# Performance work log

Measured on AMD Instinct MI355X. Metric: run time of the kernel, lower is better.

The kernel has to match this reference:

```python
import jax, jax.numpy as jnp
import numpy as np

B, K_IN, K_STATE, K_OUT = 16384, 256, 1024, 256
MEANDT = 1.0


def setup_inputs() -> dict:
    key = jax.random.key(0)
    ks = jax.random.split(key, 12)
    stdv = 1.0 / np.sqrt(K_STATE)
    u = lambda k, shape: jax.random.uniform(k, shape, jnp.float32, -stdv, stdv)
    # Lh_gate bias: second half (r-gate) initialized to -1 per init_params
    b_hg = jnp.concatenate([u(ks[6], (K_STATE,)), -jnp.ones((K_STATE,), jnp.float32)])
    return {
        "x": jax.random.normal(ks[0], (B, K_IN), jnp.float32),
        "state": jax.random.normal(ks[1], (B, K_STATE), jnp.float32),
        "dt": jnp.full((1,), 0.1, jnp.float32),
        "W_in": u(ks[2], (K_STATE, K_IN)),   # expand_input Linear weight
        "b_in": u(ks[3], (K_STATE,)),
        "W_lx": u(ks[4], (3 * K_STATE, K_STATE)),  # Lx, no bias
        "W_hg": u(ks[5], (2 * K_STATE, K_STATE)),  # Lh_gate
        "b_hg": b_hg,
        "W_hl": u(ks[7], (K_STATE, K_STATE)),      # Lh_lin
        "b_hl": u(ks[8], (K_STATE,)),
        "W_y1": u(ks[9], (K_STATE, K_STATE)),      # Ly first Linear, no bias
        "W_y2": u(ks[10], (K_OUT, K_STATE)),       # Ly second Linear, no bias
    }


def reference(x, state, dt, W_in, b_in, W_lx, W_hg, b_hg, W_hl, b_hl, W_y1, W_y2):
    dt = dt[0]

    def f(x0, h):
        # GRU-like derivative: z * (tanh(Lx_lin + Lh_lin(r*h)) - h) / meandt
        lx = x0 @ W_lx.T                       # [B, 3K]
        lh_gate = h @ W_hg.T + b_hg            # [B, 2K]
        gates = jax.nn.sigmoid(lx[:, : 2 * K_STATE] + lh_gate)
        z = gates[:, :K_STATE]
        r = gates[:, K_STATE:]
        lin = lx[:, 2 * K_STATE:] + (r * h) @ W_hl.T + b_hl
        return z * (jnp.tanh(lin) - h) / MEANDT

    # expand_input: Linear + Tanh. x_half/x_full are None -> all stages use x0.
    x0 = jnp.tanh(x @ W_in.T + b_in)           # [B, K]

    # RK4 integration
    k1 = f(x0, state)
    k2 = f(x0, state + dt * (0.5 * k1))
    k3 = f(x0, state + dt * (0.5 * k2))
    k4 = f(x0, state + dt * k3)
    state_new = state + dt * (k1 + 2 * k2 + 2 * k3 + k4) / 6  # dropout p=0 -> identity

    # Ly: Linear -> Tanh -> Linear (no biases)
    y_new = jnp.tanh(state_new @ W_y1.T) @ W_y2.T              # [B, K_OUT]
    return y_new, state_new
```

## Files before the change

### kernel.cpp

```cpp
#include <hip/hip_runtime.h>
#include <cstdint>
#include <cstddef>

#define DEVI __device__ __forceinline__

namespace {

constexpr int Bsz  = 16384;
constexpr int KIN  = 256;
constexpr int KST  = 1024;
constexpr int KOUT = 256;

typedef __bf16 bf16x8 __attribute__((ext_vector_type(8)));
typedef float  f32x4  __attribute__((ext_vector_type(4)));

DEVI float sigmoidf_(float x) { return 1.0f / (1.0f + expf(-x)); }

DEVI void gload16(const void* gsrc, void* ldst) {
    __builtin_amdgcn_global_load_lds((__attribute__((address_space(1))) void*)gsrc,
                                     (__attribute__((address_space(3))) void*)ldst,
                                     16, 0, 0);
}

DEVI void ld8f(const float* p, float* v) {
    const float4 a = *(const float4*)p;
    const float4 b = *(const float4*)(p + 4);
    v[0]=a.x; v[1]=a.y; v[2]=a.z; v[3]=a.w;
    v[4]=b.x; v[5]=b.y; v[6]=b.z; v[7]=b.w;
}
DEVI void st8f(float* p, const float* v) {
    *(float4*)p       = (float4){v[0],v[1],v[2],v[3]};
    *(float4*)(p + 4) = (float4){v[4],v[5],v[6],v[7]};
}
DEVI void ld8bf(const __bf16* p, float* v) {
    const bf16x8 o = *(const bf16x8*)p;
#pragma unroll
    for (int i = 0; i < 8; ++i) v[i] = (float)o[i];
}
DEVI void st8bf(__bf16* p, const float* v) {
    bf16x8 o;
#pragma unroll
    for (int i = 0; i < 8; ++i) o[i] = (__bf16)v[i];
    *(bf16x8*)p = o;
}
DEVI void ld8h(const float* p, float* v)  { ld8f(p, v); }
DEVI void ld8h(const __bf16* p, float* v) { ld8bf(p, v); }

struct EpX0 {
    __bf16* out; const float* bias;
    DEVI void begin() {}
    DEVI void store16(const float* v, int r, int c) {
#pragma unroll
        for (int q = 0; q < 2; ++q) {
            float b[8], o[8];
            ld8f(bias + c + q * 8, b);
#pragma unroll
            for (int e = 0; e < 8; ++e) o[e] = tanhf(v[q*8+e] + b[e]);
            st8bf(out + (size_t)r * KST + c + q * 8, o);
        }
    }
};
struct EpLx {
    __bf16* out;
    DEVI void begin() {}
    DEVI void store16(const float* v, int r, int c) {
#pragma unroll
        for (int q = 0; q < 2; ++q)
            st8bf(out + (size_t)r * (3 * KST) + c + q * 8, v + q * 8);
    }
};
template <class HT>
struct EpGates {
    __bf16* Z; __bf16* RH; const __bf16* lx; const float* bhg; const HT* h;
    DEVI void begin() {}
    DEVI void store16(const float* v, int r, int c) {
#pragma unroll
        for (int q = 0; q < 2; ++q) {
            float l[8], b[8], g[8];
            ld8bf(lx + (size_t)r * (3 * KST) + c + q * 8, l);
            ld8f(bhg + c + q * 8, b);
#pragma unroll
            for (int e = 0; e < 8; ++e) g[e] = sigmoidf_(l[e] + v[q*8+e] + b[e]);
            if (c < KST) {
                st8bf(Z + (size_t)r * KST + c + q * 8, g);
            } else {
                const size_t i = (size_t)r * KST + (c - KST) + q * 8;
                float hh[8];
                ld8h(h + i, hh);
#pragma unroll
                for (int e = 0; e < 8; ++e) g[e] *= hh[e];
                st8bf(RH + i, g);
            }
        }
    }
};
template <int STAGE, class HT>
struct EpLin {
    const __bf16* Z; const __bf16* lx; const float* bhl; const HT* h;
    const float* state; float* acc; __bf16* hn; const float* dtp;
    float dtv;
    DEVI void begin() { dtv = *dtp; }
    DEVI void store16(const float* v, int r, int c) {
#pragma unroll
        for (int q = 0; q < 2; ++q) {
            const size_t i = (size_t)r * KST + c + q * 8;
            float l[8], z[8], hh[8], st[8], b[8], kk[8], ov[8], hv[8];
            ld8bf(lx + (size_t)r * (3 * KST) + 2 * KST + c + q * 8, l);
            ld8bf(Z + i, z);
            ld8h(h + i, hh);
            ld8f(state + i, st);
            ld8f(bhl + c + q * 8, b);
#pragma unroll
            for (int e = 0; e < 8; ++e)
                kk[e] = z[e] * (tanhf(l[e] + v[q*8+e] + b[e]) - hh[e]);
            if constexpr (STAGE == 0) {
#pragma unroll
                for (int e = 0; e < 8; ++e) { ov[e] = kk[e]; hv[e] = st[e] + 0.5f * dtv * kk[e]; }
            } else if constexpr (STAGE == 1 || STAGE == 2) {
                float a[8]; ld8f(acc + i, a);
                const float hc = (STAGE == 1) ? 0.5f : 1.0f;
#pragma unroll
                for (int e = 0; e < 8; ++e) { ov[e] = a[e] + 2.f * kk[e]; hv[e] = st[e] + hc * dtv * kk[e]; }
            } else {
                float a[8]; ld8f(acc + i, a);
#pragma unroll
                for (int e = 0; e < 8; ++e) { ov[e] = st[e] + dtv * (a[e] + kk[e]) * (1.f / 6.f); hv[e] = ov[e]; }
            }
            st8f(acc + i, ov);
            st8bf(hn + i, hv);
        }
    }
};
struct EpT {
    __bf16* out;
    DEVI void begin() {}
    DEVI void store16(const float* v, int r, int c) {
#pragma unroll
        for (int q = 0; q < 2; ++q) {
            float o[8];
#pragma unroll
            for (int e = 0; e < 8; ++e) o[e] = tanhf(v[q*8+e]);
            st8bf(out + (size_t)r * KST + c + q * 8, o);
        }
    }
};
struct EpY {
    float* out;
    DEVI void begin() {}
    DEVI void store16(const float* v, int r, int c) {
        st8f(out + (size_t)r * KOUT + c, v);
        st8f(out + (size_t)r * KOUT + c + 8, v + 8);
    }
};

template <class Ep>
__global__ __launch_bounds__(256)
void gemm_bt(const __bf16* __restrict__ A, const __bf16* __restrict__ W,
             const int K, Ep ep)
{
    __shared__ __bf16 As[128 * 32];
    __shared__ __bf16 Bs[128 * 32];
    __shared__ float  bounce[32 * 132];
    const int m0 = blockIdx.x * 128;
    const int n0 = blockIdx.y * 128;
    const int t  = threadIdx.x;
    const int l  = t & 63;
    const int w  = t >> 6;
    const int wr = w >> 1;
    const int wc = w & 1;
    const int fr = l & 15;
    const int fq = l >> 4;
    const int srow = t >> 2;
    const int sk   = (t & 3) << 3;

    const __bf16* Ap0 = A + (size_t)(m0 + srow) * K + sk;
    const __bf16* Ap1 = Ap0 + (size_t)64 * K;
    const __bf16* Bp0 = W + (size_t)(n0 + srow) * K + sk;
    const __bf16* Bp1 = Bp0 + (size_t)64 * K;
    __bf16* la0 = &As[t * 8];
    __bf16* la1 = &As[2048 + t * 8];
    __bf16* lb0 = &Bs[t * 8];
    __bf16* lb1 = &Bs[2048 + t * 8];

    f32x4 acc[4][4];
#pragma unroll
    for (int i = 0; i < 4; ++i)
#pragma unroll
        for (int j = 0; j < 4; ++j) acc[i][j] = (f32x4){0.f, 0.f, 0.f, 0.f};

    for (int k0 = 0; k0 < K; k0 += 32) {
        gload16(Ap0 + k0, la0);
        gload16(Ap1 + k0, la1);
        gload16(Bp0 + k0, lb0);
        gload16(Bp1 + k0, lb1);
        __syncthreads();
        bf16x8 av[4], bv[4];
#pragma unroll
        for (int mi = 0; mi < 4; ++mi)
            av[mi] = *(const bf16x8*)&As[(wr * 64 + mi * 16 + fr) * 32 + fq * 8];
#pragma unroll
        for (int ni = 0; ni < 4; ++ni)
            bv[ni] = *(const bf16x8*)&Bs[(wc * 64 + ni * 16 + fr) * 32 + fq * 8];
#pragma unroll
        for (int mi = 0; mi < 4; ++mi)
#pragma unroll
            for (int ni = 0; ni < 4; ++ni)
                acc[mi][ni] = __builtin_amdgcn_mfma_f32_16x16x32_bf16(av[mi], bv[ni], acc[mi][ni], 0, 0, 0);
        __syncthreads();
    }

    ep.begin();
#pragma unroll
    for (int band = 0; band < 4; ++band) {
        if (wr == (band >> 1)) {
            const int mi0 = 2 * (band & 1);
#pragma unroll
            for (int mm = 0; mm < 2; ++mm)
#pragma unroll
                for (int ni = 0; ni < 4; ++ni)
#pragma unroll
                    for (int j = 0; j < 4; ++j)
                        bounce[(mm * 16 + fq * 4 + j) * 132 + wc * 64 + ni * 16 + fr]
                            = acc[mi0 + mm][ni][j];
        }
        __syncthreads();
        {
            const int r  = t >> 3;
            const int c0 = (t & 7) * 16;
            float v[16];
#pragma unroll
            for (int kk = 0; kk < 16; ++kk) v[kk] = bounce[r * 132 + c0 + kk];
            ep.store16(v, m0 + band * 32 + r, n0 + c0);
        }
        __syncthreads();
    }
}

__global__ __launch_bounds__(256)
void cvt_bf16(const float* __restrict__ s, __bf16* __restrict__ d, int n8)
{
    for (int i = blockIdx.x * blockDim.x + threadIdx.x; i < n8; i += gridDim.x * blockDim.x) {
        const float4 a = ((const float4*)s)[2 * i];
        const float4 b = ((const float4*)s)[2 * i + 1];
        bf16x8 v;
        v[0] = (__bf16)a.x; v[1] = (__bf16)a.y; v[2] = (__bf16)a.z; v[3] = (__bf16)a.w;
        v[4] = (__bf16)b.x; v[5] = (__bf16)b.y; v[6] = (__bf16)b.z; v[7] = (__bf16)b.w;
        ((bf16x8*)d)[i] = v;
    }
}

}

extern "C" void kernel_launch(void* const* d_in, const int* in_sizes, int n_in,
                              void* d_out, int out_size, void* d_ws, size_t ws_size,
                              hipStream_t stream)
{
    (void)in_sizes; (void)n_in; (void)out_size;

    const float* x     = (const float*)d_in[0];
    const float* state = (const float*)d_in[1];
    const float* dtp   = (const float*)d_in[2];
    const float* W_in  = (const float*)d_in[3];
    const float* b_in  = (const float*)d_in[4];
    const float* W_lx  = (const float*)d_in[5];
    const float* W_hg  = (const float*)d_in[6];
    const float* b_hg  = (const float*)d_in[7];
    const float* W_hl  = (const float*)d_in[8];
    const float* b_hl  = (const float*)d_in[9];
    const float* W_y1  = (const float*)d_in[10];
    const float* W_y2  = (const float*)d_in[11];

    float* y_out  = (float*)d_out;
    float* st_new = y_out + (size_t)Bsz * KOUT;

    const size_t nWin = (size_t)KST * KIN, nWlx = (size_t)3 * KST * KST,
                 nWhg = (size_t)2 * KST * KST, nWhl = (size_t)KST * KST,
                 nWy1 = (size_t)KST * KST, nWy2 = (size_t)KOUT * KST;
    const size_t fixedB = ((size_t)Bsz * KIN + 2 * (size_t)Bsz * KST
                           + nWin + nWlx + nWhg + nWhl + nWy1 + nWy2) * 2;

    int CB = 1024;
    while (CB < 8192 && fixedB + (size_t)(2 * CB) * KST * 12 <= ws_size) CB <<= 1;
    if (fixedB + (size_t)CB * KST * 12 > ws_size) return;

    uint8_t* p = (uint8_t*)d_ws;
    __bf16* x_bf  = (__bf16*)p; p += (size_t)Bsz * KIN * 2;
    __bf16* st_bf = (__bf16*)p; p += (size_t)Bsz * KST * 2;
    __bf16* snb   = (__bf16*)p; p += (size_t)Bsz * KST * 2;
    __bf16* Wb_in = (__bf16*)p; p += nWin * 2;
    __bf16* Wb_lx = (__bf16*)p; p += nWlx * 2;
    __bf16* Wb_hg = (__bf16*)p; p += nWhg * 2;
    __bf16* Wb_hl = (__bf16*)p; p += nWhl * 2;
    __bf16* Wb_y1 = (__bf16*)p; p += nWy1 * 2;
    __bf16* Wb_y2 = (__bf16*)p; p += nWy2 * 2;
    __bf16* lx    = (__bf16*)p; p += (size_t)CB * 3 * KST * 2;
    __bf16* Zb    = (__bf16*)p; p += (size_t)CB * KST * 2;
    __bf16* h_bf  = (__bf16*)p; p += (size_t)CB * KST * 2;
    __bf16* RH    = (__bf16*)p;
    __bf16* t_bf  = lx;

    const dim3 blk(256);
    auto cg = [](size_t n) { return dim3((unsigned)((n / 8 + 255) / 256 > 2048 ? 2048 : (n / 8 + 255) / 256)); };
    auto g  = [](int M, int N) { return dim3((unsigned)(M / 128), (unsigned)(N / 128)); };

    cvt_bf16<<<cg((size_t)Bsz * KIN), blk, 0, stream>>>(x, x_bf, (int)((size_t)Bsz * KIN / 8));
    cvt_bf16<<<cg((size_t)Bsz * KST), blk, 0, stream>>>(state, st_bf, (int)((size_t)Bsz * KST / 8));
    cvt_bf16<<<cg(nWin), blk, 0, stream>>>(W_in, Wb_in, (int)(nWin / 8));
    cvt_bf16<<<cg(nWlx), blk, 0, stream>>>(W_lx, Wb_lx, (int)(nWlx / 8));
    cvt_bf16<<<cg(nWhg), blk, 0, stream>>>(W_hg, Wb_hg, (int)(nWhg / 8));
    cvt_bf16<<<cg(nWhl), blk, 0, stream>>>(W_hl, Wb_hl, (int)(nWhl / 8));
    cvt_bf16<<<cg(nWy1), blk, 0, stream>>>(W_y1, Wb_y1, (int)(nWy1 / 8));
    cvt_bf16<<<cg(nWy2), blk, 0, stream>>>(W_y2, Wb_y2, (int)(nWy2 / 8));

    for (int c0 = 0; c0 < Bsz; c0 += CB) {
        const __bf16* xs  = x_bf + (size_t)c0 * KIN;
        const __bf16* ssb = st_bf + (size_t)c0 * KST;
        const float*  ss  = state + (size_t)c0 * KST;
        float*  sn   = st_new + (size_t)c0 * KST;
        __bf16* snbs = snb + (size_t)c0 * KST;

        gemm_bt<<<g(CB, KST), blk, 0, stream>>>(xs, Wb_in, KIN, EpX0{h_bf, b_in});
        gemm_bt<<<g(CB, 3 * KST), blk, 0, stream>>>(h_bf, Wb_lx, KST, EpLx{lx});

        gemm_bt<<<g(CB, 2 * KST), blk, 0, stream>>>(ssb, Wb_hg, KST, EpGates<float>{Zb, RH, lx, b_hg, ss});
        gemm_bt<<<g(CB, KST), blk, 0, stream>>>(RH, Wb_hl, KST, EpLin<0, float>{Zb, lx, b_hl, ss, ss, sn, h_bf, dtp});
        gemm_bt<<<g(CB, 2 * KST), blk, 0, stream>>>(h_bf, Wb_hg, KST, EpGates<__bf16>{Zb, RH, lx, b_hg, h_bf});
        gemm_bt<<<g(CB, KST), blk, 0, stream>>>(RH, Wb_hl, KST, EpLin<1, __bf16>{Zb, lx, b_hl, h_bf, ss, sn, h_bf, dtp});
        gemm_bt<<<g(CB, 2 * KST), blk, 0, stream>>>(h_bf, Wb_hg, KST, EpGates<__bf16>{Zb, RH, lx, b_hg, h_bf});
        gemm_bt<<<g(CB, KST), blk, 0, stream>>>(RH, Wb_hl, KST, EpLin<2, __bf16>{Zb, lx, b_hl, h_bf, ss, sn, h_bf, dtp});
        gemm_bt<<<g(CB, 2 * KST), blk, 0, stream>>>(h_bf, Wb_hg, KST, EpGates<__bf16>{Zb, RH, lx, b_hg, h_bf});
        gemm_bt<<<g(CB, KST), blk, 0, stream>>>(RH, Wb_hl, KST, EpLin<3, __bf16>{Zb, lx, b_hl, h_bf, ss, sn, snbs, dtp});
    }

    const int CBY = (4 * CB < Bsz) ? 4 * CB : Bsz;
    for (int c0 = 0; c0 < Bsz; c0 += CBY) {
        gemm_bt<<<g(CBY, KST), blk, 0, stream>>>(snb + (size_t)c0 * KST, Wb_y1, KST, EpT{t_bf});
        gemm_bt<<<g(CBY, KOUT), blk, 0, stream>>>(t_bf, Wb_y2, KST, EpY{y_out + (size_t)c0 * KOUT});
    }
}
```

Measured before the change: 1.539 ms.

## Add 256x256-tile double-buffered GEMM kernel and enlarge batch chunk size

```diff
diff --git a/kernel.cpp b/kernel.cpp
--- a/kernel.cpp
+++ b/kernel.cpp
@@ -152,6 +152,108 @@
         st8f(out + (size_t)r * KOUT + c + 8, v + 8);
     }
 };
+
+DEVI void compute_tile64(const __bf16* a, const __bf16* b,
+                         f32x4 (&acc)[8][4], int wr, int wc, int fr, int fq)
+{
+#pragma unroll
+    for (int kk = 0; kk < 2; ++kk) {
+        bf16x8 av[8], bv[4];
+#pragma unroll
+        for (int mi = 0; mi < 8; ++mi)
+            av[mi] = *(const bf16x8*)&a[(wr * 128 + mi * 16 + fr) * 64 + kk * 32 + fq * 8];
+#pragma unroll
+        for (int ni = 0; ni < 4; ++ni)
+            bv[ni] = *(const bf16x8*)&b[(wc * 64 + ni * 16 + fr) * 64 + kk * 32 + fq * 8];
+#pragma unroll
+        for (int mi = 0; mi < 8; ++mi)
+#pragma unroll
+            for (int ni = 0; ni < 4; ++ni)
+                acc[mi][ni] = __builtin_amdgcn_mfma_f32_16x16x32_bf16(av[mi], bv[ni], acc[mi][ni], 0, 0, 0);
+    }
+}
+
+template <class Ep>
+__global__ __launch_bounds__(512, 2)
+void gemm_bt2(const __bf16* __restrict__ A, const __bf16* __restrict__ W,
+              const int K, Ep ep)
+{
+    __shared__ __bf16 sm[4][256 * 64];
+    const int m0 = blockIdx.x * 256;
+    const int n0 = blockIdx.y * 256;
+    const int t  = threadIdx.x;
+    const int l  = t & 63;
+    const int w  = t >> 6;
+    const int wr = w >> 2;
+    const int wc = w & 3;
+    const int fr = l & 15;
+    const int fq = l >> 4;
+    const int srow = t >> 3;
+    const int scol = (t & 7) << 3;
+
+    const __bf16* Ap = A + (size_t)(m0 + srow) * K + scol;
+    const __bf16* Bp = W + (size_t)(n0 + srow) * K + scol;
+
+    f32x4 acc[8][4];
+#pragma unroll
+    for (int i = 0; i < 8; ++i)
+#pragma unroll
+        for (int j = 0; j < 4; ++j) acc[i][j] = (f32x4){0.f, 0.f, 0.f, 0.f};
+
+    const int NT = K >> 6;
+
+#define STAGE_KT(buf, kt)                                                     \
+    {                                                                         \
+        const int k0_ = (kt) << 6;                                            \
+        __bf16* da_ = &sm[(buf) * 2 + 0][t * 8];                              \
+        __bf16* db_ = &sm[(buf) * 2 + 1][t * 8];                              \
+        _Pragma("unroll")                                                     \
+        for (int q = 0; q < 4; ++q) {                                         \
+            gload16(Ap + (size_t)(q * 64) * K + k0_, da_ + q * 4096);         \
+            gload16(Bp + (size_t)(q * 64) * K + k0_, db_ + q * 4096);         \
+        }                                                                     \
+    }
+
+    STAGE_KT(0, 0);
+    __syncthreads();
+    int cur = 0;
+    for (int kt = 0; kt < NT - 1; ++kt) {
+        STAGE_KT(cur ^ 1, kt + 1);
+        compute_tile64(sm[cur * 2 + 0], sm[cur * 2 + 1], acc, wr, wc, fr, fq);
+        __syncthreads();
+        cur ^= 1;
+    }
+    compute_tile64(sm[cur * 2 + 0], sm[cur * 2 + 1], acc, wr, wc, fr, fq);
+    __syncthreads();
+#undef STAGE_KT
+
+    float* bounce = (float*)&sm[0][0];
+    ep.begin();
+#pragma unroll
+    for (int band = 0; band < 8; ++band) {
+        if (wr == (band >> 2)) {
+            const int mi0 = 2 * (band & 3);
+#pragma unroll
+            for (int mm = 0; mm < 2; ++mm)
+#pragma unroll
+                for (int ni = 0; ni < 4; ++ni)
+#pragma unroll
+                    for (int j = 0; j < 4; ++j)
+                        bounce[(mm * 16 + fq * 4 + j) * 258 + wc * 64 + ni * 16 + fr]
+                            = acc[mi0 + mm][ni][j];
+        }
+        __syncthreads();
+        {
+            const int r  = t >> 4;
+            const int c0 = (t & 15) * 16;
+            float v[16];
+#pragma unroll
+            for (int k2 = 0; k2 < 16; ++k2) v[k2] = bounce[r * 258 + c0 + k2];
+            ep.store16(v, m0 + band * 32 + r, n0 + c0);
+        }
+        __syncthreads();
+    }
+}
 
 template <class Ep>
 __global__ __launch_bounds__(256)
@@ -280,7 +382,7 @@
                            + nWin + nWlx + nWhg + nWhl + nWy1 + nWy2) * 2;
 
     int CB = 1024;
-    while (CB < 8192 && fixedB + (size_t)(2 * CB) * KST * 12 <= ws_size) CB <<= 1;
+    while (CB < Bsz && fixedB + (size_t)(2 * CB) * KST * 12 <= ws_size) CB <<= 1;
     if (fixedB + (size_t)CB * KST * 12 > ws_size) return;
 
     uint8_t* p = (uint8_t*)d_ws;
@@ -299,9 +401,10 @@
     __bf16* RH    = (__bf16*)p;
     __bf16* t_bf  = lx;
 
-    const dim3 blk(256);
+    const dim3 blk(256), blk2(512);
     auto cg = [](size_t n) { return dim3((unsigned)((n / 8 + 255) / 256 > 2048 ? 2048 : (n / 8 + 255) / 256)); };
-    auto g  = [](int M, int N) { return dim3((unsigned)(M / 128), (unsigned)(N / 128)); };
+    auto g1 = [](int M, int N) { return dim3((unsigned)(M / 128), (unsigned)(N / 128)); };
+    auto g2 = [](int M, int N) { return dim3((unsigned)(M / 256), (unsigned)(N / 256)); };
 
     cvt_bf16<<<cg((size_t)Bsz * KIN), blk, 0, stream>>>(x, x_bf, (int)((size_t)Bsz * KIN / 8));
     cvt_bf16<<<cg((size_t)Bsz * KST), blk, 0, stream>>>(state, st_bf, (int)((size_t)Bsz * KST / 8));
@@ -319,22 +422,22 @@
         float*  sn   = st_new + (size_t)c0 * KST;
         __bf16* snbs = snb + (size_t)c0 * KST;
 
-        gemm_bt<<<g(CB, KST), blk, 0, stream>>>(xs, Wb_in, KIN, EpX0{h_bf, b_in});
-        gemm_bt<<<g(CB, 3 * KST), blk, 0, stream>>>(h_bf, Wb_lx, KST, EpLx{lx});
-
-        gemm_bt<<<g(CB, 2 * KST), blk, 0, stream>>>(ssb, Wb_hg, KST, EpGates<float>{Zb, RH, lx, b_hg, ss});
-        gemm_bt<<<g(CB, KST), blk, 0, stream>>>(RH, Wb_hl, KST, EpLin<0, float>{Zb, lx, b_hl, ss, ss, sn, h_bf, dtp});
-        gemm_bt<<<g(CB, 2 * KST), blk, 0, stream>>>(h_bf, Wb_hg, KST, EpGates<__bf16>{Zb, RH, lx, b_hg, h_bf});
-        gemm_bt<<<g(CB, KST), blk, 0, stream>>>(RH, Wb_hl, KST, EpLin<1, __bf16>{Zb, lx, b_hl, h_bf, ss, sn, h_bf, dtp});
-        gemm_bt<<<g(CB, 2 * KST), blk, 0, stream>>>(h_bf, Wb_hg, KST, EpGates<__bf16>{Zb, RH, lx, b_hg, h_bf});
-        gemm_bt<<<g(CB, KST), blk, 0, stream>>>(RH, Wb_hl, KST, EpLin<2, __bf16>{Zb, lx, b_hl, h_bf, ss, sn, h_bf, dtp});
-        gemm_bt<<<g(CB, 2 * KST), blk, 0, stream>>>(h_bf, Wb_hg, KST, EpGates<__bf16>{Zb, RH, lx, b_hg, h_bf});
-        gemm_bt<<<g(CB, KST), blk, 0, stream>>>(RH, Wb_hl, KST, EpLin<3, __bf16>{Zb, lx, b_hl, h_bf, ss, sn, snbs, dtp});
+        gemm_bt2<<<g2(CB, KST), blk2, 0, stream>>>(xs, Wb_in, KIN, EpX0{h_bf, b_in});
+        gemm_bt2<<<g2(CB, 3 * KST), blk2, 0, stream>>>(h_bf, Wb_lx, KST, EpLx{lx});
+
+        gemm_bt2<<<g2(CB, 2 * KST), blk2, 0, stream>>>(ssb, Wb_hg, KST, EpGates<float>{Zb, RH, lx, b_hg, ss});
+        gemm_bt2<<<g2(CB, KST), blk2, 0, stream>>>(RH, Wb_hl, KST, EpLin<0, float>{Zb, lx, b_hl, ss, ss, sn, h_bf, dtp});
+        gemm_bt2<<<g2(CB, 2 * KST), blk2, 0, stream>>>(h_bf, Wb_hg, KST, EpGates<__bf16>{Zb, RH, lx, b_hg, h_bf});
+        gemm_bt2<<<g2(CB, KST), blk2, 0, stream>>>(RH, Wb_hl, KST, EpLin<1, __bf16>{Zb, lx, b_hl, h_bf, ss, sn, h_bf, dtp});
+        gemm_bt2<<<g2(CB, 2 * KST), blk2, 0, stream>>>(h_bf, Wb_hg, KST, EpGates<__bf16>{Zb, RH, lx, b_hg, h_bf});
+        gemm_bt2<<<g2(CB, KST), blk2, 0, stream>>>(RH, Wb_hl, KST, EpLin<2, __bf16>{Zb, lx, b_hl, h_bf, ss, sn, h_bf, dtp});
+        gemm_bt2<<<g2(CB, 2 * KST), blk2, 0, stream>>>(h_bf, Wb_hg, KST, EpGates<__bf16>{Zb, RH, lx, b_hg, h_bf});
+        gemm_bt2<<<g2(CB, KST), blk2, 0, stream>>>(RH, Wb_hl, KST, EpLin<3, __bf16>{Zb, lx, b_hl, h_bf, ss, sn, snbs, dtp});
     }
 
     const int CBY = (4 * CB < Bsz) ? 4 * CB : Bsz;
     for (int c0 = 0; c0 < Bsz; c0 += CBY) {
-        gemm_bt<<<g(CBY, KST), blk, 0, stream>>>(snb + (size_t)c0 * KST, Wb_y1, KST, EpT{t_bf});
-        gemm_bt<<<g(CBY, KOUT), blk, 0, stream>>>(t_bf, Wb_y2, KST, EpY{y_out + (size_t)c0 * KOUT});
-    }
-}
+        gemm_bt2<<<g2(CBY, KST), blk2, 0, stream>>>(snb + (size_t)c0 * KST, Wb_y1, KST, EpT{t_bf});
+        gemm_bt<<<g1(CBY, KOUT), blk, 0, stream>>>(t_bf, Wb_y2, KST, EpY{y_out + (size_t)c0 * KOUT});
+    }
+}
```

Measured after the change: 1.337 ms. -13.2%, faster.
